# Performance work log

Hardware: AMD Instinct MI355X
Metric: run time of the kernel (lower is better)

The kernel has to match this reference:

```python
import jax, jax.numpy as jnp
import numpy as np

B, S, E, A = 32, 1000, 1024, 512


def setup_inputs() -> dict:
    key = jax.random.key(0)
    ks = jax.random.split(key, 7)
    sc = 0.02
    return {
        "x": jax.random.normal(ks[0], (B, S, E), dtype=jnp.float32),
        "Wk": jax.random.normal(ks[1], (E, A), dtype=jnp.float32) * sc,
        "bk": jax.random.normal(ks[2], (A,), dtype=jnp.float32) * sc,
        "Wq": jax.random.normal(ks[3], (E, A), dtype=jnp.float32) * sc,
        "bq": jax.random.normal(ks[4], (A,), dtype=jnp.float32) * sc,
        "Wv": jax.random.normal(ks[5], (E, A), dtype=jnp.float32) * sc,
        "bv": jax.random.normal(ks[6], (A,), dtype=jnp.float32) * sc,
    }


def reference(x, Wk, bk, Wq, bq, Wv, bv):
    seq = x.shape[1]
    k = x @ Wk + bk          # [B,S,A]
    q = x @ Wq + bq          # [B,S,A]
    v = x @ Wv + bv          # [B,S,A]
    # NOTE: module scales by sqrt(sequence), not sqrt(attention_dim)
    den = jnp.asarray(seq, x.dtype) ** 0.5
    scores = jnp.einsum("bqa,bka->bqk", q, k) / den  # [B,S,S]
    causal = jnp.tril(jnp.ones((seq, seq), dtype=bool))
    scores = jnp.where(causal, scores, -jnp.inf)
    attn = jax.nn.softmax(scores, axis=-1)
    return jnp.einsum("bqk,bka->bqa", attn, v)      # [B,S,A]
```

## Files before the change

kernel.cpp:

```cpp
#include <hip/hip_runtime.h>
#include <hip/hip_bf16.h>
#include <stdint.h>

#define DEVI __device__ __forceinline__

typedef short s16x8 __attribute__((ext_vector_type(8)));
typedef short s16x4 __attribute__((ext_vector_type(4)));
typedef float f32x4 __attribute__((ext_vector_type(4)));

static constexpr int BB = 32, SS = 1000, EE = 1024, AA = 512;
static constexpr int MM = BB * SS;

static constexpr size_t OFF_X16 = 0;
static constexpr size_t OFF_Q   = OFF_X16 + (size_t)MM * EE * 2;
static constexpr size_t OFF_K   = OFF_Q  + (size_t)MM * AA * 2;
static constexpr size_t OFF_VT  = OFF_K  + (size_t)MM * AA * 2;
static constexpr size_t OFF_WT  = OFF_VT + (size_t)BB * AA * SS * 2;

static constexpr int PROWS = BB * 3 * 128;
static constexpr size_t ML_OFF = (size_t)2 * PROWS * 512;

DEVI unsigned short f2bf(float f) {
  union { float f; unsigned int u; } c; c.f = f;
  unsigned int u = c.u + 0x7fffu + ((c.u >> 16) & 1u);
  return (unsigned short)(u >> 16);
}

DEVI void gl_lds16(const void* g, void* l) {
  __builtin_amdgcn_global_load_lds(
      (const __attribute__((address_space(1))) unsigned int*)g,
      (__attribute__((address_space(3))) unsigned int*)l, 16, 0, 0);
}

DEVI void wg_barrier() {
  asm volatile("" ::: "memory");
  __builtin_amdgcn_s_barrier();
  asm volatile("" ::: "memory");
}

DEVI float fast_exp2(float x) {
#if __has_builtin(__builtin_amdgcn_exp2f)
  return __builtin_amdgcn_exp2f(x);
#else
  return __builtin_exp2f(x);
#endif
}

__global__ __launch_bounds__(256) void x_to_bf16_kernel(const float* __restrict__ x,
                                                        unsigned short* __restrict__ x16) {
  const long n4 = (long)MM * EE / 4;
  long i = (long)blockIdx.x * blockDim.x + threadIdx.x;
  const long stride = (long)gridDim.x * blockDim.x;
  for (; i < n4; i += stride) {
    const float4 v = ((const float4*)x)[i];
    ushort4 o;
    o.x = f2bf(v.x); o.y = f2bf(v.y); o.z = f2bf(v.z); o.w = f2bf(v.w);
    ((ushort4*)x16)[i] = o;
  }
}

__global__ __launch_bounds__(256) void wt_kernel(const float* __restrict__ Wq,
                                                 const float* __restrict__ Wk,
                                                 const float* __restrict__ Wv,
                                                 unsigned short* __restrict__ WT) {
  const float* W = (blockIdx.z == 0) ? Wq : (blockIdx.z == 1) ? Wk : Wv;
  unsigned short* out = WT + (size_t)blockIdx.z * AA * EE;
  __shared__ unsigned short t[64][65];
  const int k0 = blockIdx.x * 64, n0 = blockIdx.y * 64;
  #pragma unroll
  for (int i = 0; i < 16; ++i) {
    int idx = i * 256 + threadIdx.x;
    int r = idx >> 6, c = idx & 63;
    t[r][c] = f2bf(W[(size_t)(k0 + r) * AA + n0 + c]);
  }
  __syncthreads();
  #pragma unroll
  for (int i = 0; i < 16; ++i) {
    int idx = i * 256 + threadIdx.x;
    int r = idx >> 6, c = idx & 63;
    out[(size_t)(n0 + r) * EE + k0 + c] = t[c][r];
  }
}

#define PROJ_PHASE4(BUF, QA, SKT, SWHa, SWHb, SBUF, DOVM)                      \
  {                                                                            \
    if ((QA) == 0) {                                                           \
      _Pragma("unroll") for (int kk = 0; kk < 2; ++kk) {                       \
        _Pragma("unroll") for (int g2 = 0; g2 < 4; ++g2) {                     \
          int row = wn * 64 + g2 * 16 + (lane & 15);                           \
          int cb = (kk * 64 + (lane >> 4) * 16) ^ ((row & 7) << 4);            \
          bR[kk][g2] = *(const s16x8*)(lds + 65536 + (BUF) * 32768 + row * 128 + cb); \
        }                                                                      \
      }                                                                        \
    }                                                                          \
    _Pragma("unroll") for (int kk = 0; kk < 2; ++kk) {                         \
      _Pragma("unroll") for (int f = 0; f < 4; ++f) {                          \
        int row = wm * 128 + ((QA) * 4 + f) * 16 + (lane & 15);                \
        int cb = (kk * 64 + (lane >> 4) * 16) ^ ((row & 7) << 4);              \
        aR[kk][f] = *(const s16x8*)(lds + (BUF) * 32768 + row * 128 + cb);     \
      }                                                                        \
    }                                                                          \
    if ((SKT) >= 0) { stage_half(SBUF, SKT, SWHa); stage_half(SBUF, SKT, SWHb); } \
    wg_barrier();                                                              \
    __builtin_amdgcn_s_setprio(1);                                             \
    _Pragma("unroll") for (int kk = 0; kk < 2; ++kk) {                         \
      _Pragma("unroll") for (int f = 0; f < 4; ++f) {                          \
        _Pragma("unroll") for (int g2 = 0; g2 < 4; ++g2) {                     \
          acc[(QA) * 4 + f][g2] = __builtin_amdgcn_mfma_f32_16x16x32_bf16(     \
              aR[kk][f], bR[kk][g2], acc[(QA) * 4 + f][g2], 0, 0, 0);          \
        }                                                                      \
      }                                                                        \
    }                                                                          \
    __builtin_amdgcn_s_setprio(0);                                             \
    if (DOVM) asm volatile("s_waitcnt vmcnt(0)" ::: "memory");                 \
    wg_barrier();                                                              \
  }

__global__ __launch_bounds__(512, 2) void proj_kernel(
    const unsigned short* __restrict__ X16, const unsigned short* __restrict__ WT,
    const float* __restrict__ bq, const float* __restrict__ bk, const float* __restrict__ bv,
    unsigned short* __restrict__ Qo, unsigned short* __restrict__ Ko,
    unsigned short* __restrict__ VTo) {
  __shared__ unsigned char lds[131072];
  const int tid = threadIdx.x, lane = tid & 63, wave = tid >> 6;
  const int wm = wave >> 2, wn = wave & 3;

  const int phys = blockIdx.x;
  int p, r;
  if (phys < 720) { int g = phys / 48, w = phys % 48; p = g * 8 + (w & 7); r = w >> 3; }
  else            { int w = phys - 720; p = 120 + w % 5; r = w / 5; }
  const int z = r >> 1, nidx = r & 1;
  const int m0 = p * 256, n0 = nidx * 256;
  const unsigned short* Wz = WT + (size_t)z * AA * EE;

  f32x4 acc[8][4];
  #pragma unroll
  for (int i = 0; i < 8; ++i)
    #pragma unroll
    for (int j = 0; j < 4; ++j) acc[i][j] = f32x4{0.f, 0.f, 0.f, 0.f};

  unsigned int offH[2];
  #pragma unroll
  for (int i = 0; i < 2; ++i) {
    int c = i * 512 + tid;
    int rl = c >> 3, s = c & 7;
    int cb = (s * 16) ^ ((rl & 7) << 4);
    offH[i] = (unsigned)(rl * EE + (cb >> 1));
  }
  auto stage_half = [&](int buf, int kt, int which) {
    const int h = which & 1;
    const int isB = which >> 1;
    const unsigned short* srcb = isB ? (Wz + (size_t)(n0 + h * 128) * EE + kt * 64)
                                     : (X16 + (size_t)(m0 + h * 128) * EE + kt * 64);
    unsigned char* dstb = lds + (isB ? 65536 : 0) + buf * 32768 + h * 16384;
    #pragma unroll
    for (int i = 0; i < 2; ++i)
      gl_lds16(srcb + offH[i], dstb + (i * 512 + tid) * 16);
  };

  stage_half(0, 0, 0); stage_half(0, 0, 1); stage_half(0, 0, 2); stage_half(0, 0, 3);
  asm volatile("s_waitcnt vmcnt(0)" ::: "memory");
  wg_barrier();

  s16x8 aR[2][4];
  s16x8 bR[2][4];
  for (int J = 0; J < 8; ++J) {
    const int t1 = 2 * J + 1;
    const int t2 = (J < 7) ? (2 * J + 2) : -1;
    PROJ_PHASE4(0, 0, t1, 0, 1, 1, false)
    PROJ_PHASE4(0, 1, t1, 2, 3, 1, true)
    PROJ_PHASE4(1, 0, t2, 0, 1, 0, false)
    PROJ_PHASE4(1, 1, t2, 2, 3, 0, true)
  }

  const float* bias = (z == 0) ? bq : (z == 1) ? bk : bv;
  const float scale = (z == 0) ? 0.04562280215f : 1.0f;
  unsigned short* T = (unsigned short*)lds;
  float bv4[4];
  #pragma unroll
  for (int nf = 0; nf < 4; ++nf) bv4[nf] = bias[n0 + wn * 64 + nf * 16 + (lane & 15)];

  if (z != 2) {
    unsigned short* O = (z == 0) ? Qo : Ko;
    #pragma unroll
    for (int h = 0; h < 2; ++h) {
      if (wm == h) {
        #pragma unroll
        for (int mf = 0; mf < 8; ++mf)
          #pragma unroll
          for (int nf = 0; nf < 4; ++nf) {
            const int col = wn * 64 + nf * 16 + (lane & 15);
            #pragma unroll
            for (int j = 0; j < 4; ++j) {
              const int rr = mf * 16 + (lane >> 4) * 4 + j;
              T[rr * 264 + col] = f2bf((acc[mf][nf][j] + bv4[nf]) * scale);
            }
          }
      }
      wg_barrier();
      #pragma unroll
      for (int i = 0; i < 8; ++i) {
        int c2 = i * 512 + tid;
        int rr = c2 >> 5, ch = (c2 & 31) * 8;
        s16x8 chunk = *(const s16x8*)&T[rr * 264 + ch];
        *(s16x8*)&O[(size_t)(m0 + h * 128 + rr) * AA + n0 + ch] = chunk;
      }
      wg_barrier();
    }
  } else {
    #pragma unroll
    for (int h = 0; h < 2; ++h) {
      if ((wn >> 1) == h) {
        #pragma unroll
        for (int mf = 0; mf < 8; ++mf)
          #pragma unroll
          for (int nf = 0; nf < 4; ++nf) {
            const int al = (wn & 1) * 64 + nf * 16 + (lane & 15);
            #pragma unroll
            for (int j = 0; j < 4; ++j) {
              const int sl = wm * 128 + mf * 16 + (lane >> 4) * 4 + j;
              T[al * 264 + sl] = f2bf(acc[mf][nf][j] + bv4[nf]);
            }
          }
      }
      wg_barrier();
      #pragma unroll
      for (int i = 0; i < 8; ++i) {
        int c2 = i * 512 + tid;
        int rr = c2 >> 5, ch = (c2 & 31) * 8;
        s16x8 chunk = *(const s16x8*)&T[rr * 264 + ch];
        const int rowg0 = m0 + ch;
        const int bb2 = rowg0 / SS, ss2 = rowg0 - bb2 * SS;
        *(s16x8*)&VTo[(size_t)bb2 * AA * SS + (size_t)(n0 + h * 128 + rr) * SS + ss2] = chunk;
      }
      wg_barrier();
    }
  }
}

__global__ __launch_bounds__(512, 2) void attn_kernel(
    const unsigned short* __restrict__ Qs, const unsigned short* __restrict__ Ks,
    const unsigned short* __restrict__ VT, float* __restrict__ out,
    float* __restrict__ part) {
  constexpr int KVB = 32;
  __shared__ unsigned char ldsK[2][KVB * AA * 2];
  __shared__ unsigned char ldsV[2][AA * KVB * 2];
  __shared__ unsigned char ldsP[8][16 * 80];

  const int tid = threadIdx.x, lane = tid & 63, wave = tid >> 6;
  const int L = blockIdx.x;
  const int b = L & 31;
  const int g = 7 - (L >> 5);

  const unsigned short* kbase = Ks + (size_t)b * SS * AA;
  const unsigned short* vbase = VT + (size_t)b * AA * SS;
  unsigned int koff[4], voff[4];
  #pragma unroll
  for (int i = 0; i < 4; ++i) {
    int c = i * 512 + tid;
    int r = c >> 6;
    int cb = ((c & 63) * 16) ^ ((r & 7) << 4);
    koff[i] = r * AA + (cb >> 1);
    int pair = c >> 3;
    int within = (c & 7) * 16;
    int half = within >> 6;
    int kb = (within & 63) ^ ((pair & 3) << 4);
    int a_ = pair * 2 + half;
    voff[i] = a_ * SS + (kb >> 1);
  }

  auto stageKV = [&](int buf, int t) {
    #pragma unroll
    for (int i = 0; i < 4; ++i)
      gl_lds16(kbase + koff[i] + (unsigned)(t * (KVB * AA)),
               &ldsK[buf][(i * 512 + tid) * 16]);
    #pragma unroll
    for (int i = 0; i < 4; ++i)
      gl_lds16(vbase + voff[i] + (unsigned)(t * KVB),
               &ldsV[buf][(i * 512 + tid) * 16]);
  };

  int ownN = 4 * (g + 1);
  int rb_[2], t0_[2], t1_[2], md_[2], cx_[2];
  int nph = 1;
  rb_[0] = 128 * g; t0_[0] = 0; t1_[0] = (ownN < 20) ? ownN : 20;
  md_[0] = (g <= 4) ? 0 : 1; cx_[0] = g - 5;
  if (g <= 2) {
    int r = 7 - g;
    rb_[1] = 128 * r; t0_[1] = 20; t1_[1] = 4 * (r + 1); md_[1] = 2; cx_[1] = r - 5;
    nph = 2;
  }

  for (int ph = 0; ph < nph; ++ph) {
    const int rowbase = rb_[ph], tbeg = t0_[ph], tend = t1_[ph];
    const int mode = md_[ph], cidx = cx_[ph];
    const int q0w = rowbase + wave * 16;

    s16x8 qf[16];
    {
      int qrow = q0w + (lane & 15);
      int qr = qrow < SS ? qrow : SS - 1;
      const unsigned short* qp = Qs + (size_t)(b * SS + qr) * AA + (lane >> 4) * 8;
      #pragma unroll
      for (int f = 0; f < 16; ++f) qf[f] = *(const s16x8*)(qp + f * 32);
    }

    f32x4 o[32];
    #pragma unroll
    for (int n = 0; n < 32; ++n) o[n] = f32x4{0.f, 0.f, 0.f, 0.f};
    float mrun[4], ps[4];
    #pragma unroll
    for (int j = 0; j < 4; ++j) { mrun[j] = -__builtin_inff(); ps[j] = 0.f; }

    stageKV(0, tbeg);
    asm volatile("s_waitcnt vmcnt(0)" ::: "memory");
    wg_barrier();

    for (int t = tbeg; t < tend; ++t) {
      const int cur = (t - tbeg) & 1;
      const int k0 = t * KVB;
      if (t + 1 < tend) stageKV(cur ^ 1, t + 1);

      f32x4 p0a = {0.f, 0.f, 0.f, 0.f}, p0b = {0.f, 0.f, 0.f, 0.f};
      f32x4 p1a = {0.f, 0.f, 0.f, 0.f}, p1b = {0.f, 0.f, 0.f, 0.f};
      {
        const int r0 = lane & 15;
        const int sw = (r0 & 7) << 4;
        const int kb16 = (lane >> 4) * 16;
        const int rb0 = r0 << 10, rb1 = (r0 + 16) << 10;
        #pragma unroll
        for (int f = 0; f < 8; ++f) {
          const int offA = f * 64 + kb16;
          const int offB = (f + 8) * 64 + kb16;
          s16x8 k0A = *(const s16x8*)&ldsK[cur][rb0 + (offA ^ sw)];
          s16x8 k1A = *(const s16x8*)&ldsK[cur][rb1 + (offA ^ sw)];
          s16x8 k0B = *(const s16x8*)&ldsK[cur][rb0 + (offB ^ sw)];
          s16x8 k1B = *(const s16x8*)&ldsK[cur][rb1 + (offB ^ sw)];
          p0a = __builtin_amdgcn_mfma_f32_16x16x32_bf16(qf[f], k0A, p0a, 0, 0, 0);
          p1a = __builtin_amdgcn_mfma_f32_16x16x32_bf16(qf[f], k1A, p1a, 0, 0, 0);
          p0b = __builtin_amdgcn_mfma_f32_16x16x32_bf16(qf[f + 8], k0B, p0b, 0, 0, 0);
          p1b = __builtin_amdgcn_mfma_f32_16x16x32_bf16(qf[f + 8], k1B, p1b, 0, 0, 0);
        }
      }
      f32x4 p0 = p0a + p0b, p1 = p1a + p1b;

      const int kcol = k0 + (lane & 15);
      float lm[4];
      #pragma unroll
      for (int j = 0; j < 4; ++j) {
        const int q = q0w + (lane >> 4) * 4 + j;
        float s0 = p0[j], s1 = p1[j];
        if (kcol > q || kcol >= SS) s0 = -__builtin_inff();
        if (kcol + 16 > q || kcol + 16 >= SS) s1 = -__builtin_inff();
        p0[j] = s0; p1[j] = s1;
        lm[j] = fmaxf(s0, s1);
      }
      const int myneed = (lm[0] > mrun[0] + 8.f) | (lm[1] > mrun[1] + 8.f) |
                         (lm[2] > mrun[2] + 8.f) | (lm[3] > mrun[3] + 8.f);
      if (__any(myneed)) {
        float rm[4] = {lm[0], lm[1], lm[2], lm[3]};
        #pragma unroll
        for (int st = 1; st <= 8; st <<= 1)
          #pragma unroll
          for (int j = 0; j < 4; ++j) rm[j] = fmaxf(rm[j], __shfl_xor(rm[j], st));
        float corr[4];
        #pragma unroll
        for (int j = 0; j < 4; ++j) {
          const float mnew = fmaxf(mrun[j], rm[j]);
          corr[j] = fast_exp2(mrun[j] - mnew);
          mrun[j] = mnew;
          ps[j] *= corr[j];
        }
        #pragma unroll
        for (int n = 0; n < 32; ++n)
          #pragma unroll
          for (int j = 0; j < 4; ++j) o[n][j] *= corr[j];
      }
      #pragma unroll
      for (int j = 0; j < 4; ++j) {
        const float e0 = fast_exp2(p0[j] - mrun[j]);
        const float e1 = fast_exp2(p1[j] - mrun[j]);
        ps[j] += e0 + e1;
        p0[j] = e0; p1[j] = e1;
      }

      {
        unsigned short* pb = (unsigned short*)&ldsP[wave][0];
        const int prow = (lane >> 4) * 4, pc = lane & 15;
        #pragma unroll
        for (int j = 0; j < 4; ++j) {
          pb[(prow + j) * 40 + pc]      = f2bf(p0[j]);
          pb[(prow + j) * 40 + pc + 16] = f2bf(p1[j]);
        }
      }
      s16x8 pa;
      {
        const unsigned char* pp = &ldsP[wave][(lane & 15) * 80 + (lane >> 4) * 16];
        s16x4 lo = *(const s16x4*)pp;
        s16x4 hi = *(const s16x4*)(pp + 8);
        pa = s16x8{lo[0], lo[1], lo[2], lo[3], hi[0], hi[1], hi[2], hi[3]};
      }

      #pragma unroll
      for (int n = 0; n < 32; ++n) {
        const int a_ = n * 16 + (lane & 15);
        const int pair = a_ >> 1;
        const int off = pair * 128 + (a_ & 1) * 64 + (((lane >> 4) * 16) ^ ((pair & 3) << 4));
        s16x8 vb = *(const s16x8*)&ldsV[cur][off];
        o[n] = __builtin_amdgcn_mfma_f32_16x16x32_bf16(pa, vb, o[n], 0, 0, 0);
      }

      asm volatile("s_waitcnt vmcnt(0)" ::: "memory");
      wg_barrier();
    }

    #pragma unroll
    for (int st = 1; st <= 8; st <<= 1)
      #pragma unroll
      for (int j = 0; j < 4; ++j) ps[j] += __shfl_xor(ps[j], st);

    if (mode == 0) {
      #pragma unroll
      for (int j = 0; j < 4; ++j) {
        const int q = q0w + (lane >> 4) * 4 + j;
        if (q < SS) {
          const float inv = 1.0f / ps[j];
          float* op = out + (size_t)(b * SS + q) * AA + (lane & 15);
          #pragma unroll
          for (int n = 0; n < 32; ++n) op[n * 16] = o[n][j] * inv;
        }
      }
    } else {
      const int slot = mode - 1;
      #pragma unroll
      for (int j = 0; j < 4; ++j) {
        const int rl = wave * 16 + (lane >> 4) * 4 + j;
        const size_t idx = (size_t)slot * PROWS + ((size_t)(b * 3 + cidx) * 128 + rl);
        float* po = part + idx * 512 + (lane & 15);
        #pragma unroll
        for (int n = 0; n < 32; ++n) po[n * 16] = o[n][j];
        if ((lane & 15) == 0) {
          float* pml = part + ML_OFF + idx * 2;
          pml[0] = mrun[j];
          pml[1] = ps[j];
        }
      }
    }
  }
}

__global__ __launch_bounds__(256) void combine_kernel(const float* __restrict__ part,
                                                      float* __restrict__ out) {
  const int rid = blockIdx.x * 2 + (threadIdx.x >> 7);
  const int t = threadIdx.x & 127;
  const int b = rid / 384;
  const int rem = rid - b * 384;
  const int c = rem >> 7, row = rem & 127;
  const int q = (c + 5) * 128 + row;
  if (q >= SS) return;
  const float* mlA = part + ML_OFF + (size_t)rid * 2;
  const float* mlB = part + ML_OFF + ((size_t)PROWS + rid) * 2;
  const float mA = mlA[0], lA = mlA[1];
  const float mB = mlB[0], lB = mlB[1];
  const float m = fmaxf(mA, mB);
  const float sA = fast_exp2(mA - m), sB = fast_exp2(mB - m);
  const float inv = 1.0f / (lA * sA + lB * sB);
  const float4 a = ((const float4*)(part + (size_t)rid * 512))[t];
  const float4 d = ((const float4*)(part + ((size_t)PROWS + rid) * 512))[t];
  float4 r;
  r.x = (a.x * sA + d.x * sB) * inv;
  r.y = (a.y * sA + d.y * sB) * inv;
  r.z = (a.z * sA + d.z * sB) * inv;
  r.w = (a.w * sA + d.w * sB) * inv;
  ((float4*)(out + ((size_t)b * SS + q) * AA))[t] = r;
}

extern "C" void kernel_launch(void* const* d_in, const int* in_sizes, int n_in,
                              void* d_out, int out_size, void* d_ws, size_t ws_size,
                              hipStream_t stream) {
  const float* x  = (const float*)d_in[0];
  const float* Wk = (const float*)d_in[1];
  const float* bk = (const float*)d_in[2];
  const float* Wq = (const float*)d_in[3];
  const float* bq = (const float*)d_in[4];
  const float* Wv = (const float*)d_in[5];
  const float* bv = (const float*)d_in[6];

  char* ws = (char*)d_ws;
  unsigned short* X16 = (unsigned short*)(ws + OFF_X16);
  unsigned short* Qw  = (unsigned short*)(ws + OFF_Q);
  unsigned short* Kw  = (unsigned short*)(ws + OFF_K);
  unsigned short* VTw = (unsigned short*)(ws + OFF_VT);
  unsigned short* WT  = (unsigned short*)(ws + OFF_WT);
  float* Part = (float*)(ws + OFF_X16);

  x_to_bf16_kernel<<<dim3(2048), dim3(256), 0, stream>>>(x, X16);
  wt_kernel<<<dim3(EE / 64, AA / 64, 3), dim3(256), 0, stream>>>(Wq, Wk, Wv, WT);
  proj_kernel<<<dim3(750), dim3(512), 0, stream>>>(
      X16, WT, bq, bk, bv, Qw, Kw, VTw);
  attn_kernel<<<dim3(256), dim3(512), 0, stream>>>(Qw, Kw, VTw, (float*)d_out, Part);
  combine_kernel<<<dim3(PROWS / 2), dim3(256), 0, stream>>>(Part, (float*)d_out);
}
```

Baseline: 277.1 us.

## Rebalance causal attention split across more row blocks and store partials in bf16

Changes the split-K schedule for the causal attention so four row-block pairs are split at tile 18 instead of three at tile 20. Each workgroup then does a more even share of key tiles, which shortens the longest workgroup. Partial outputs are now written as bf16 instead of fp32, halving partial-buffer traffic in both the attention and combine kernels. The mask value moves from -inf to a large finite negative. The cost is more combine work, one extra partial row block per batch, and some precision lost in the bf16 partials.

```diff
diff --git a/kernel.cpp b/kernel.cpp
--- a/kernel.cpp
+++ b/kernel.cpp
@@ -17,13 +17,20 @@
 static constexpr size_t OFF_VT  = OFF_K  + (size_t)MM * AA * 2;
 static constexpr size_t OFF_WT  = OFF_VT + (size_t)BB * AA * SS * 2;
 
-static constexpr int PROWS = BB * 3 * 128;
-static constexpr size_t ML_OFF = (size_t)2 * PROWS * 512;
+static constexpr int PROWS = BB * 4 * 128;
+static constexpr size_t PART_O_ELEMS = (size_t)2 * PROWS * 512;
+static constexpr int KSPLIT_T = 18;
+#define MNEG (-3.0e38f)
 
 DEVI unsigned short f2bf(float f) {
   union { float f; unsigned int u; } c; c.f = f;
   unsigned int u = c.u + 0x7fffu + ((c.u >> 16) & 1u);
   return (unsigned short)(u >> 16);
+}
+
+DEVI float bf2f(unsigned short h) {
+  union { unsigned int u; float f; } c; c.u = ((unsigned int)h) << 16;
+  return c.f;
 }
 
 DEVI void gl_lds16(const void* g, void* l) {
@@ -241,7 +248,7 @@
 __global__ __launch_bounds__(512, 2) void attn_kernel(
     const unsigned short* __restrict__ Qs, const unsigned short* __restrict__ Ks,
     const unsigned short* __restrict__ VT, float* __restrict__ out,
-    float* __restrict__ part) {
+    unsigned short* __restrict__ partO, float* __restrict__ partML) {
   constexpr int KVB = 32;
   __shared__ unsigned char ldsK[2][KVB * AA * 2];
   __shared__ unsigned char ldsV[2][AA * KVB * 2];
@@ -283,11 +290,11 @@
   int ownN = 4 * (g + 1);
   int rb_[2], t0_[2], t1_[2], md_[2], cx_[2];
   int nph = 1;
-  rb_[0] = 128 * g; t0_[0] = 0; t1_[0] = (ownN < 20) ? ownN : 20;
-  md_[0] = (g <= 4) ? 0 : 1; cx_[0] = g - 5;
-  if (g <= 2) {
+  rb_[0] = 128 * g; t0_[0] = 0; t1_[0] = (ownN < KSPLIT_T) ? ownN : KSPLIT_T;
+  md_[0] = (g <= 3) ? 0 : 1; cx_[0] = g - 4;
+  if (g <= 3) {
     int r = 7 - g;
-    rb_[1] = 128 * r; t0_[1] = 20; t1_[1] = 4 * (r + 1); md_[1] = 2; cx_[1] = r - 5;
+    rb_[1] = 128 * r; t0_[1] = KSPLIT_T; t1_[1] = 4 * (r + 1); md_[1] = 2; cx_[1] = r - 4;
     nph = 2;
   }
 
@@ -310,7 +317,7 @@
     for (int n = 0; n < 32; ++n) o[n] = f32x4{0.f, 0.f, 0.f, 0.f};
     float mrun[4], ps[4];
     #pragma unroll
-    for (int j = 0; j < 4; ++j) { mrun[j] = -__builtin_inff(); ps[j] = 0.f; }
+    for (int j = 0; j < 4; ++j) { mrun[j] = MNEG; ps[j] = 0.f; }
 
     stageKV(0, tbeg);
     asm volatile("s_waitcnt vmcnt(0)" ::: "memory");
@@ -350,8 +357,8 @@
       for (int j = 0; j < 4; ++j) {
         const int q = q0w + (lane >> 4) * 4 + j;
         float s0 = p0[j], s1 = p1[j];
-        if (kcol > q || kcol >= SS) s0 = -__builtin_inff();
-        if (kcol + 16 > q || kcol + 16 >= SS) s1 = -__builtin_inff();
+        if (kcol > q || kcol >= SS) s0 = MNEG;
+        if (kcol + 16 > q || kcol + 16 >= SS) s1 = MNEG;
         p0[j] = s0; p1[j] = s1;
         lm[j] = fmaxf(s0, s1);
       }
@@ -435,12 +442,12 @@
       #pragma unroll
       for (int j = 0; j < 4; ++j) {
         const int rl = wave * 16 + (lane >> 4) * 4 + j;
-        const size_t idx = (size_t)slot * PROWS + ((size_t)(b * 3 + cidx) * 128 + rl);
-        float* po = part + idx * 512 + (lane & 15);
-        #pragma unroll
-        for (int n = 0; n < 32; ++n) po[n * 16] = o[n][j];
+        const size_t idx = (size_t)slot * PROWS + ((size_t)(b * 4 + cidx) * 128 + rl);
+        unsigned short* po = partO + idx * 512 + (lane & 15);
+        #pragma unroll
+        for (int n = 0; n < 32; ++n) po[n * 16] = f2bf(o[n][j]);
         if ((lane & 15) == 0) {
-          float* pml = part + ML_OFF + idx * 2;
+          float* pml = partML + idx * 2;
           pml[0] = mrun[j];
           pml[1] = ps[j];
         }
@@ -449,29 +456,30 @@
   }
 }
 
-__global__ __launch_bounds__(256) void combine_kernel(const float* __restrict__ part,
+__global__ __launch_bounds__(256) void combine_kernel(const unsigned short* __restrict__ partO,
+                                                      const float* __restrict__ partML,
                                                       float* __restrict__ out) {
   const int rid = blockIdx.x * 2 + (threadIdx.x >> 7);
   const int t = threadIdx.x & 127;
-  const int b = rid / 384;
-  const int rem = rid - b * 384;
+  const int b = rid >> 9;
+  const int rem = rid & 511;
   const int c = rem >> 7, row = rem & 127;
-  const int q = (c + 5) * 128 + row;
+  const int q = (c + 4) * 128 + row;
   if (q >= SS) return;
-  const float* mlA = part + ML_OFF + (size_t)rid * 2;
-  const float* mlB = part + ML_OFF + ((size_t)PROWS + rid) * 2;
+  const float* mlA = partML + (size_t)rid * 2;
+  const float* mlB = partML + ((size_t)PROWS + rid) * 2;
   const float mA = mlA[0], lA = mlA[1];
   const float mB = mlB[0], lB = mlB[1];
   const float m = fmaxf(mA, mB);
   const float sA = fast_exp2(mA - m), sB = fast_exp2(mB - m);
   const float inv = 1.0f / (lA * sA + lB * sB);
-  const float4 a = ((const float4*)(part + (size_t)rid * 512))[t];
-  const float4 d = ((const float4*)(part + ((size_t)PROWS + rid) * 512))[t];
+  const ushort4 ua = ((const ushort4*)(partO + (size_t)rid * 512))[t];
+  const ushort4 ud = ((const ushort4*)(partO + ((size_t)PROWS + rid) * 512))[t];
   float4 r;
-  r.x = (a.x * sA + d.x * sB) * inv;
-  r.y = (a.y * sA + d.y * sB) * inv;
-  r.z = (a.z * sA + d.z * sB) * inv;
-  r.w = (a.w * sA + d.w * sB) * inv;
+  r.x = (bf2f(ua.x) * sA + bf2f(ud.x) * sB) * inv;
+  r.y = (bf2f(ua.y) * sA + bf2f(ud.y) * sB) * inv;
+  r.z = (bf2f(ua.z) * sA + bf2f(ud.z) * sB) * inv;
+  r.w = (bf2f(ua.w) * sA + bf2f(ud.w) * sB) * inv;
   ((float4*)(out + ((size_t)b * SS + q) * AA))[t] = r;
 }
 
@@ -492,12 +500,14 @@
   unsigned short* Kw  = (unsigned short*)(ws + OFF_K);
   unsigned short* VTw = (unsigned short*)(ws + OFF_VT);
   unsigned short* WT  = (unsigned short*)(ws + OFF_WT);
-  float* Part = (float*)(ws + OFF_X16);
+  unsigned short* PartO = (unsigned short*)(ws + OFF_X16);
+  float* PartML = (float*)(ws + OFF_X16 + PART_O_ELEMS * 2);
 
   x_to_bf16_kernel<<<dim3(2048), dim3(256), 0, stream>>>(x, X16);
   wt_kernel<<<dim3(EE / 64, AA / 64, 3), dim3(256), 0, stream>>>(Wq, Wk, Wv, WT);
   proj_kernel<<<dim3(750), dim3(512), 0, stream>>>(
       X16, WT, bq, bk, bv, Qw, Kw, VTw);
-  attn_kernel<<<dim3(256), dim3(512), 0, stream>>>(Qw, Kw, VTw, (float*)d_out, Part);
-  combine_kernel<<<dim3(PROWS / 2), dim3(256), 0, stream>>>(Part, (float*)d_out);
-}
+  attn_kernel<<<dim3(256), dim3(512), 0, stream>>>(Qw, Kw, VTw, (float*)d_out,
+                                                   PartO, PartML);
+  combine_kernel<<<dim3(PROWS / 2), dim3(256), 0, stream>>>(PartO, PartML, (float*)d_out);
+}
```

After: 276.0 us. Within noise of the previous version (-0.4%).
